# Optimization experiments

Measured on AMD Instinct MI355X. Metric: run time of the kernel, lower is better.

## Reference

```python
import jax, jax.numpy as jnp
import numpy as np

B, T, C, H, N = 4, 4096, 1024, 16, 64
D_DECAY, D_AAA, D_MV, D_GATE = 64, 64, 32, 160
EPS_GN = 1e-5 * 8 ** 2  # GroupNorm eps = 1e-5 * head_size_divisor**2


def _k(i):
    return jax.random.fold_in(jax.random.key(0), i)


def setup_inputs():
    p = {}
    p["x"] = jax.random.normal(_k(1), (B, T, C), jnp.float32)
    p["v_first"] = jax.random.normal(_k(2), (B, T, C), jnp.float32)
    for i, name in enumerate(["x_r", "x_w", "x_k", "x_v", "x_a", "x_g"]):
        p[name] = jax.random.uniform(_k(10 + i), (1, 1, C), jnp.float32)
    p["w0"] = jnp.linspace(-7.0, -2.0, C, dtype=jnp.float32).reshape(1, 1, C) + 0.5
    p["w1"] = jax.random.normal(_k(20), (C, D_DECAY), jnp.float32) * 0.02
    p["w2"] = jax.random.normal(_k(21), (D_DECAY, C), jnp.float32) * 0.02
    p["a0"] = jax.random.normal(_k(22), (1, 1, C), jnp.float32) * 0.02
    p["a1"] = jax.random.normal(_k(23), (C, D_AAA), jnp.float32) * 0.02
    p["a2"] = jax.random.normal(_k(24), (D_AAA, C), jnp.float32) * 0.02
    p["v0"] = jnp.ones((1, 1, C), jnp.float32)
    p["v1"] = jax.random.normal(_k(25), (C, D_MV), jnp.float32) * 0.02
    p["v2"] = jax.random.normal(_k(26), (D_MV, C), jnp.float32) * 0.02
    p["g1"] = jax.random.normal(_k(27), (C, D_GATE), jnp.float32) * 0.02
    p["g2"] = jax.random.normal(_k(28), (D_GATE, C), jnp.float32) * 0.02
    p["k_k"] = jnp.full((1, 1, C), 0.85, jnp.float32)
    p["k_a"] = jnp.ones((1, 1, C), jnp.float32)
    p["r_k"] = jax.random.normal(_k(29), (H, N), jnp.float32) * 0.02
    s = 0.5 / C ** 0.5
    p["Wr"] = jax.random.uniform(_k(30), (C, C), jnp.float32, -s, s)
    p["Wk"] = jax.random.uniform(_k(31), (C, C), jnp.float32, -0.1 * s, 0.1 * s)
    p["Wv"] = jax.random.uniform(_k(32), (C, C), jnp.float32, -s, s)
    p["Wo"] = jax.random.uniform(_k(33), (C, C), jnp.float32, -s, s)
    p["ln_w"] = jnp.ones((C,), jnp.float32)
    p["ln_b"] = jnp.zeros((C,), jnp.float32)
    p["alpha"] = jnp.array(0.5, jnp.float32)
    return p


def _wkv_scan(ins, reverse):
    # ins: tuple of time-major (T,B,H,N) arrays: r, decay, k, v, a, b
    def step(S, inp):
        r_t, d_t, k_t, v_t, a_t, b_t = inp
        sa = jnp.einsum('bhij,bhj->bhi', S, a_t)  # in-context removal term
        S = (S * d_t[:, :, None, :]
             + sa[..., None] * b_t[:, :, None, :]
             + v_t[..., None] * k_t[:, :, None, :])
        return S, jnp.einsum('bhij,bhj->bhi', S, r_t)
    S0 = jnp.zeros((B, H, N, N), jnp.float32)
    return jax.lax.scan(step, S0, ins, reverse=reverse)[1]


def reference(x, v_first, x_r, x_w, x_k, x_v, x_a, x_g, w0, w1, w2, a0, a1, a2,
              v0, v1, v2, g1, g2, k_k, k_a, r_k, Wr, Wk, Wv, Wo, ln_w, ln_b, alpha):
    xx = jnp.pad(x, ((0, 0), (1, 0), (0, 0)))[:, :T, :] - x  # token shift
    xr = x + xx * x_r
    xw = x + xx * x_w
    xk = x + xx * x_k
    xv = x + xx * x_v
    xa = x + xx * x_a
    xg = x + xx * x_g
    r = xr @ Wr.T
    w = -jax.nn.softplus(-(w0 + jnp.tanh(xw @ w1) @ w2)) - 0.5
    k = xk @ Wk.T
    v = xv @ Wv.T
    v = v + (v_first - v) * jax.nn.sigmoid(v0 + (xv @ v1) @ v2)  # layer_id != 0
    a = jax.nn.sigmoid(a0 + (xa @ a1) @ a2)
    g = jax.nn.sigmoid(xg @ g1) @ g2
    kk = (k * k_k).reshape(B, T, H, N)
    kk = kk / jnp.maximum(jnp.linalg.norm(kk, axis=-1, keepdims=True), 1e-12)
    k = k * (1.0 + (a - 1.0) * k_a)
    rh = r.reshape(B, T, H, N)
    kh = k.reshape(B, T, H, N)
    vh = v.reshape(B, T, H, N)
    dec = jnp.exp(-jnp.exp(w.reshape(B, T, H, N)))  # per-channel decay
    ah = -kk
    bh = kk * a.reshape(B, T, H, N)
    tm = lambda z: jnp.transpose(z, (1, 0, 2, 3))  # -> (T,B,H,N)
    ins = (tm(rh), tm(dec), tm(kh), tm(vh), tm(ah), tm(bh))
    y_f = _wkv_scan(ins, reverse=False)
    y_b = _wkv_scan(ins, reverse=True)
    y = alpha * y_f + (1.0 - alpha) * y_b  # bidirectional blend (alpha)
    y = jnp.transpose(y, (1, 0, 2, 3))  # (B,T,H,N)
    mu = y.mean(-1, keepdims=True)
    var = y.var(-1, keepdims=True)
    y = (y - mu) / jnp.sqrt(var + EPS_GN)  # GroupNorm(H groups)
    y = y * ln_w.reshape(1, 1, H, N) + ln_b.reshape(1, 1, H, N)
    y = y + (rh * kh * r_k).sum(-1, keepdims=True) * vh
    out = (y.reshape(B, T, C) * g) @ Wo.T
    return (out, v_first)
```

## Files before the change

kernel.cpp:

```cpp
#include <hip/hip_runtime.h>
#include <hip/hip_bf16.h>
#include <math.h>

#define BB 4
#define TT 4096
#define CC 1024
#define HH 16
#define NN 64
#define BT (BB*TT)
#define EPS_GN 6.4e-4f
#define TMAX (TT-1)
#define LCH 64
#define CB 8
#define NB 8
#define STR 68
#define STR2 36

typedef __attribute__((ext_vector_type(8))) short bf16x8;
typedef __attribute__((ext_vector_type(4))) float f32x4;

__device__ __forceinline__ float sigmoidf_(float x) {
    return 1.0f / (1.0f + expf(-x));
}

__device__ __forceinline__ float waveReduceSum(float v) {
    #pragma unroll
    for (int off = 32; off > 0; off >>= 1)
        v += __shfl_xor(v, off, 64);
    return v;
}

__device__ __forceinline__ unsigned short f2bf(float f) {
    unsigned u = __float_as_uint(f);
    u += 0x7FFFu + ((u >> 16) & 1u);
    return (unsigned short)(u >> 16);
}
__device__ __forceinline__ float bf2f(unsigned short h) {
    return __uint_as_float(((unsigned)h) << 16);
}

__device__ __forceinline__ void gll16(const unsigned short* g, unsigned short* l) {
    __builtin_amdgcn_global_load_lds(
        (__attribute__((address_space(1))) void*)(g),
        (__attribute__((address_space(3))) void*)(l), 16, 0, 0);
}

template<int SA0,int SA1,int SB0,int SB1>
__device__ __forceinline__ void gemm64(const float* __restrict__ A,
                                       const float* __restrict__ B,
                                       float acc[4][4], int tr, int tc) {
    #pragma unroll 2
    for (int kx = 0; kx < 64; kx += 4) {
        float a_[4][4];
        if (SA0 == 1) {
            #pragma unroll
            for (int kk = 0; kk < 4; kk++) {
                float4 t = *(const float4*)&A[tr + (kx + kk) * SA1];
                a_[0][kk] = t.x; a_[1][kk] = t.y; a_[2][kk] = t.z; a_[3][kk] = t.w;
            }
        } else {
            #pragma unroll
            for (int r = 0; r < 4; r++) {
                float4 t = *(const float4*)&A[(tr + r) * SA0 + kx];
                a_[r][0] = t.x; a_[r][1] = t.y; a_[r][2] = t.z; a_[r][3] = t.w;
            }
        }
        float b_[4][4];
        if (SB0 == 1) {
            #pragma unroll
            for (int kk = 0; kk < 4; kk++) {
                float4 t = *(const float4*)&B[tc + (kx + kk) * SB1];
                b_[0][kk] = t.x; b_[1][kk] = t.y; b_[2][kk] = t.z; b_[3][kk] = t.w;
            }
        } else {
            #pragma unroll
            for (int cq = 0; cq < 4; cq++) {
                float4 t = *(const float4*)&B[(tc + cq) * SB0 + kx];
                b_[cq][0] = t.x; b_[cq][1] = t.y; b_[cq][2] = t.z; b_[cq][3] = t.w;
            }
        }
        #pragma unroll
        for (int r = 0; r < 4; r++)
            #pragma unroll
            for (int cq = 0; cq < 4; cq++)
                #pragma unroll
                for (int kk = 0; kk < 4; kk++)
                    acc[r][cq] = fmaf(a_[r][kk], b_[cq][kk], acc[r][cq]);
    }
}

__global__ __launch_bounds__(256) void conv_split_x3(
    const float* __restrict__ X,
    const float* __restrict__ mr, const float* __restrict__ mk,
    const float* __restrict__ mv,
    unsigned short* __restrict__ rH, unsigned short* __restrict__ rL,
    unsigned short* __restrict__ kH, unsigned short* __restrict__ kL,
    unsigned short* __restrict__ vH, unsigned short* __restrict__ vL)
{
    int g = blockIdx.x * 256 + threadIdx.x;
    int m = g >> 7;
    int k = (g & 127) * 8;
    const float* px = X + (size_t)m * CC + k;
    float xv8[8], pv[8];
    {
        float4 x0 = *(const float4*)px;
        float4 x1 = *(const float4*)(px + 4);
        xv8[0]=x0.x; xv8[1]=x0.y; xv8[2]=x0.z; xv8[3]=x0.w;
        xv8[4]=x1.x; xv8[5]=x1.y; xv8[6]=x1.z; xv8[7]=x1.w;
    }
    if ((m & (TT - 1)) == 0) {
        #pragma unroll
        for (int j = 0; j < 8; j++) pv[j] = 0.f;
    } else {
        float4 p0 = *(const float4*)(px - CC);
        float4 p1 = *(const float4*)(px - CC + 4);
        pv[0]=p0.x; pv[1]=p0.y; pv[2]=p0.z; pv[3]=p0.w;
        pv[4]=p1.x; pv[5]=p1.y; pv[6]=p1.z; pv[7]=p1.w;
    }
    const float* mixes[3] = {mr, mk, mv};
    unsigned short* His[3] = {rH, kH, vH};
    unsigned short* Los[3] = {rL, kL, vL};
    #pragma unroll
    for (int s = 0; s < 3; s++) {
        float4 m0 = *(const float4*)(mixes[s] + k);
        float4 m1 = *(const float4*)(mixes[s] + k + 4);
        float mv8[8] = {m0.x,m0.y,m0.z,m0.w,m1.x,m1.y,m1.z,m1.w};
        unsigned short hi[8], lo[8];
        #pragma unroll
        for (int j = 0; j < 8; j++) {
            float a = xv8[j] + (pv[j] - xv8[j]) * mv8[j];
            hi[j] = f2bf(a);
            lo[j] = f2bf(a - bf2f(hi[j]));
        }
        uint4 H, L;
        H.x = (unsigned)hi[0] | ((unsigned)hi[1] << 16);
        H.y = (unsigned)hi[2] | ((unsigned)hi[3] << 16);
        H.z = (unsigned)hi[4] | ((unsigned)hi[5] << 16);
        H.w = (unsigned)hi[6] | ((unsigned)hi[7] << 16);
        L.x = (unsigned)lo[0] | ((unsigned)lo[1] << 16);
        L.y = (unsigned)lo[2] | ((unsigned)lo[3] << 16);
        L.z = (unsigned)lo[4] | ((unsigned)lo[5] << 16);
        L.w = (unsigned)lo[6] | ((unsigned)lo[7] << 16);
        *(uint4*)(His[s] + (size_t)g * 8) = H;
        *(uint4*)(Los[s] + (size_t)g * 8) = L;
    }
}

__global__ __launch_bounds__(256) void conv_w4(
    const float* __restrict__ Wr, const float* __restrict__ Wk,
    const float* __restrict__ Wv, const float* __restrict__ Wo,
    unsigned short* __restrict__ Hi, unsigned short* __restrict__ Lo)
{
    int g = blockIdx.x * 256 + threadIdx.x;
    int y = blockIdx.y;
    const float* W = (y == 0) ? Wr : (y == 1) ? Wk : (y == 2) ? Wv : Wo;
    size_t doff = (size_t)y * CC * CC;
    int m = g >> 7;
    int k = (g & 127) * 8;
    const float* px = W + (size_t)m * CC + k;
    float a[8];
    {
        float4 x0 = *(const float4*)px;
        float4 x1 = *(const float4*)(px + 4);
        a[0]=x0.x; a[1]=x0.y; a[2]=x0.z; a[3]=x0.w;
        a[4]=x1.x; a[5]=x1.y; a[6]=x1.z; a[7]=x1.w;
    }
    unsigned short hi[8], lo[8];
    #pragma unroll
    for (int j = 0; j < 8; j++) {
        hi[j] = f2bf(a[j]);
        lo[j] = f2bf(a[j] - bf2f(hi[j]));
    }
    uint4 H, L;
    H.x = (unsigned)hi[0] | ((unsigned)hi[1] << 16);
    H.y = (unsigned)hi[2] | ((unsigned)hi[3] << 16);
    H.z = (unsigned)hi[4] | ((unsigned)hi[5] << 16);
    H.w = (unsigned)hi[6] | ((unsigned)hi[7] << 16);
    L.x = (unsigned)lo[0] | ((unsigned)lo[1] << 16);
    L.y = (unsigned)lo[2] | ((unsigned)lo[3] << 16);
    L.z = (unsigned)lo[4] | ((unsigned)lo[5] << 16);
    L.w = (unsigned)lo[6] | ((unsigned)lo[7] << 16);
    *(uint4*)(Hi + doff + (size_t)g * 8) = H;
    *(uint4*)(Lo + doff + (size_t)g * 8) = L;
}

__global__ __launch_bounds__(256) void conv_w2(
    const float* __restrict__ W, int K, int Kp,
    unsigned short* __restrict__ Hi, unsigned short* __restrict__ Lo)
{
    int idx = blockIdx.x * 256 + threadIdx.x;
    int nk8 = Kp >> 3;
    if (idx >= CC * nk8) return;
    int n = idx / nk8, k0 = (idx - n * nk8) * 8;
    unsigned short h8[8], l8[8];
    #pragma unroll
    for (int j = 0; j < 8; j++) {
        int k = k0 + j;
        float v = (k < K) ? W[(size_t)k * CC + n] : 0.f;
        h8[j] = f2bf(v);
        l8[j] = f2bf(v - bf2f(h8[j]));
    }
    uint4 H, L;
    H.x = (unsigned)h8[0] | ((unsigned)h8[1] << 16);
    H.y = (unsigned)h8[2] | ((unsigned)h8[3] << 16);
    H.z = (unsigned)h8[4] | ((unsigned)h8[5] << 16);
    H.w = (unsigned)h8[6] | ((unsigned)h8[7] << 16);
    L.x = (unsigned)l8[0] | ((unsigned)l8[1] << 16);
    L.y = (unsigned)l8[2] | ((unsigned)l8[3] << 16);
    L.z = (unsigned)l8[4] | ((unsigned)l8[5] << 16);
    L.w = (unsigned)l8[6] | ((unsigned)l8[7] << 16);
    *(uint4*)(Hi + (size_t)n * Kp + k0) = H;
    *(uint4*)(Lo + (size_t)n * Kp + k0) = L;
}

__global__ __launch_bounds__(256, 3) void gemm_split_bf16(
    const unsigned short* __restrict__ A0h, const unsigned short* __restrict__ A0l,
    const unsigned short* __restrict__ A1h, const unsigned short* __restrict__ A1l,
    const unsigned short* __restrict__ A2h, const unsigned short* __restrict__ A2l,
    const unsigned short* __restrict__ W4h, const unsigned short* __restrict__ W4l,
    float* __restrict__ O0, float* __restrict__ O1, float* __restrict__ O2,
    int wbase)
{
    __shared__ __align__(16) unsigned short lds[4][128 * 32];
    const int sel = blockIdx.y;
    const unsigned short* Ah = (sel == 0) ? A0h : (sel == 1) ? A1h : A2h;
    const unsigned short* Al = (sel == 0) ? A0l : (sel == 1) ? A1l : A2l;
    float* Out = (sel == 0) ? O0 : (sel == 1) ? O1 : O2;
    const unsigned short* Bh = W4h + (size_t)(wbase + sel) * CC * CC;
    const unsigned short* Bl = W4l + (size_t)(wbase + sel) * CC * CC;
    const int tid = threadIdx.x, lane = tid & 63, wave = tid >> 6;
    const int wm = (wave >> 1) * 64, wn = (wave & 1) * 64;
    const int wg = blockIdx.x;
    const int xcd = wg & 7;
    const int j = wg >> 3;
    const int m0 = ((j >> 3) * 8 + xcd) * 128;
    const int n0 = (j & 7) * 128;

    f32x4 acc[4][4];
    #pragma unroll
    for (int i = 0; i < 4; i++)
        #pragma unroll
        for (int jj = 0; jj < 4; jj++)
            acc[i][jj] = (f32x4){0.f, 0.f, 0.f, 0.f};

    for (int k0 = 0; k0 < CC; k0 += 32) {
        #pragma unroll
        for (int p = 0; p < 4; p++) {
            const unsigned short* sbase = (p == 0) ? Ah : (p == 1) ? Al
                                        : (p == 2) ? Bh : Bl;
            const int rbase = (p < 2) ? m0 : n0;
            #pragma unroll
            for (int i = 0; i < 2; i++) {
                int slot = i * 256 + wave * 64 + lane;
                int row = slot >> 2, gsl = slot & 3;
                const unsigned short* src = sbase
                    + (size_t)(rbase + row) * CC + k0 + ((gsl ^ (row & 3)) * 8);
                gll16(src, &lds[p][(size_t)(i * 256 + wave * 64) * 8]);
            }
        }
        __syncthreads();

        const int gk = lane >> 4;
        bf16x8 bhf[4], blf[4];
        #pragma unroll
        for (int nt = 0; nt < 4; nt++) {
            int col = wn + nt * 16 + (lane & 15);
            int el = col * 32 + ((gk ^ (col & 3)) * 8);
            bhf[nt] = *(const bf16x8*)&lds[2][el];
            blf[nt] = *(const bf16x8*)&lds[3][el];
        }
        #pragma unroll
        for (int mt = 0; mt < 4; mt++) {
            int row = wm + mt * 16 + (lane & 15);
            int el = row * 32 + ((gk ^ (row & 3)) * 8);
            bf16x8 ahf = *(const bf16x8*)&lds[0][el];
            bf16x8 alf = *(const bf16x8*)&lds[1][el];
            #pragma unroll
            for (int nt = 0; nt < 4; nt++) {
                acc[mt][nt] = __builtin_amdgcn_mfma_f32_16x16x32_bf16(
                    ahf, bhf[nt], acc[mt][nt], 0, 0, 0);
                acc[mt][nt] = __builtin_amdgcn_mfma_f32_16x16x32_bf16(
                    alf, bhf[nt], acc[mt][nt], 0, 0, 0);
                acc[mt][nt] = __builtin_amdgcn_mfma_f32_16x16x32_bf16(
                    ahf, blf[nt], acc[mt][nt], 0, 0, 0);
            }
        }
        __syncthreads();
    }
    #pragma unroll
    for (int mt = 0; mt < 4; mt++)
        #pragma unroll
        for (int nt = 0; nt < 4; nt++) {
            int col = n0 + wn + nt * 16 + (lane & 15);
            #pragma unroll
            for (int r = 0; r < 4; r++) {
                int row = m0 + wm + mt * 16 + (lane >> 4) * 4 + r;
                Out[(size_t)row * CC + col] = acc[mt][nt][r];
            }
        }
}

__global__ __launch_bounds__(256) void lora1_all(
    const float* __restrict__ X,
    const float* __restrict__ w1, const float* __restrict__ a1,
    const float* __restrict__ v1, const float* __restrict__ g1,
    const float* __restrict__ xw, const float* __restrict__ xa,
    const float* __restrict__ xv, const float* __restrict__ xg,
    unsigned short* __restrict__ awh, unsigned short* __restrict__ awl,
    unsigned short* __restrict__ aah, unsigned short* __restrict__ aal,
    unsigned short* __restrict__ avh, unsigned short* __restrict__ avl,
    unsigned short* __restrict__ agh, unsigned short* __restrict__ agl)
{
    const int y = blockIdx.y;
    const float* W; const float* mix; unsigned short *Hi, *Lo;
    int Ncols, n0, epi, Kp;
    if (y == 0)      { W=w1; mix=xw; Hi=awh; Lo=awl; Ncols=64;  n0=0;          epi=1; Kp=64;  }
    else if (y == 1) { W=a1; mix=xa; Hi=aah; Lo=aal; Ncols=64;  n0=0;          epi=0; Kp=64;  }
    else if (y == 2) { W=v1; mix=xv; Hi=avh; Lo=avl; Ncols=32;  n0=0;          epi=0; Kp=64;  }
    else             { W=g1; mix=xg; Hi=agh; Lo=agl; Ncols=160; n0=(y-3)*64;   epi=2; Kp=192; }

    __shared__ float As[8][64];
    __shared__ float Bs[8][64];
    const int tid = threadIdx.x;
    const int m0 = blockIdx.x * 64;
    const int sr  = tid >> 1;
    const int skq = (tid & 1) * 4;
    const int t2  = tid - 128;
    const int bkr = t2 >> 4;
    const int bnq = (t2 & 15) * 4;
    const int tm = (tid >> 3) * 2;
    const int tn = (tid & 7) * 8;

    float acc[2][8];
    #pragma unroll
    for (int i = 0; i < 2; i++)
        #pragma unroll
        for (int j = 0; j < 8; j++) acc[i][j] = 0.f;

    auto ldAm = [&](int gm, int gk) -> float4 {
        const float* px = X + (size_t)gm * CC + gk;
        float4 xvv = *(const float4*)px;
        float4 pv;
        if ((gm & (TT - 1)) == 0) pv = make_float4(0.f, 0.f, 0.f, 0.f);
        else pv = *(const float4*)(px - CC);
        float4 mv = *(const float4*)(mix + gk);
        xvv.x += (pv.x - xvv.x) * mv.x;
        xvv.y += (pv.y - xvv.y) * mv.y;
        xvv.z += (pv.z - xvv.z) * mv.z;
        xvv.w += (pv.w - xvv.w) * mv.w;
        return xvv;
    };

    float4 aR = make_float4(0.f, 0.f, 0.f, 0.f);
    float4 bR = make_float4(0.f, 0.f, 0.f, 0.f);
    if (tid < 128) {
        aR = ldAm(m0 + sr, skq);
    } else {
        int gn = n0 + bnq;
        bR = (gn < Ncols) ? *(const float4*)(W + (size_t)bkr * Ncols + gn)
                          : make_float4(0.f, 0.f, 0.f, 0.f);
    }

    for (int k0 = 0; k0 < CC; k0 += 8) {
        __syncthreads();
        if (tid < 128) {
            As[skq + 0][sr] = aR.x;
            As[skq + 1][sr] = aR.y;
            As[skq + 2][sr] = aR.z;
            As[skq + 3][sr] = aR.w;
        } else {
            *(float4*)&Bs[bkr][bnq] = bR;
        }
        __syncthreads();

        if (k0 + 8 < CC) {
            if (tid < 128) {
                aR = ldAm(m0 + sr, k0 + 8 + skq);
            } else {
                int gn = n0 + bnq;
                bR = (gn < Ncols) ? *(const float4*)(W + (size_t)(k0 + 8 + bkr) * Ncols + gn)
                                  : make_float4(0.f, 0.f, 0.f, 0.f);
            }
        }

        #pragma unroll
        for (int kk = 0; kk < 8; ++kk) {
            float av[2], bv[8];
            av[0] = As[kk][tm];
            av[1] = As[kk][tm + 1];
            *(float4*)&bv[0] = *(const float4*)&Bs[kk][tn];
            *(float4*)&bv[4] = *(const float4*)&Bs[kk][tn + 4];
            #pragma unroll
            for (int i = 0; i < 2; i++)
                #pragma unroll
                for (int j = 0; j < 8; j++)
                    acc[i][j] = fmaf(av[i], bv[j], acc[i][j]);
        }
    }

    #pragma unroll
    for (int i = 0; i < 2; i++) {
        int gm = m0 + tm + i;
        int gn = n0 + tn;
        if (gn < Kp) {
            unsigned short h8[8], l8[8];
            #pragma unroll
            for (int j = 0; j < 8; j++) {
                float v = 0.f;
                if (gn + j < Ncols) {
                    v = acc[i][j];
                    if (epi == 1) v = tanhf(v);
                    else if (epi == 2) v = sigmoidf_(v);
                }
                h8[j] = f2bf(v);
                l8[j] = f2bf(v - bf2f(h8[j]));
            }
            uint4 H, L;
            H.x = (unsigned)h8[0] | ((unsigned)h8[1] << 16);
            H.y = (unsigned)h8[2] | ((unsigned)h8[3] << 16);
            H.z = (unsigned)h8[4] | ((unsigned)h8[5] << 16);
            H.w = (unsigned)h8[6] | ((unsigned)h8[7] << 16);
            L.x = (unsigned)l8[0] | ((unsigned)l8[1] << 16);
            L.y = (unsigned)l8[2] | ((unsigned)l8[3] << 16);
            L.z = (unsigned)l8[4] | ((unsigned)l8[5] << 16);
            L.w = (unsigned)l8[6] | ((unsigned)l8[7] << 16);
            *(uint4*)(Hi + (size_t)gm * Kp + gn) = H;
            *(uint4*)(Lo + (size_t)gm * Kp + gn) = L;
        }
    }
}

__global__ __launch_bounds__(256, 3) void lora2_mfma(
    const unsigned short* __restrict__ awh, const unsigned short* __restrict__ awl,
    const unsigned short* __restrict__ aah, const unsigned short* __restrict__ aal,
    const unsigned short* __restrict__ avh, const unsigned short* __restrict__ avl,
    const unsigned short* __restrict__ agh, const unsigned short* __restrict__ agl,
    const unsigned short* __restrict__ w2h, const unsigned short* __restrict__ w2l,
    const unsigned short* __restrict__ a2h, const unsigned short* __restrict__ a2l,
    const unsigned short* __restrict__ v2h, const unsigned short* __restrict__ v2l,
    const unsigned short* __restrict__ g2h, const unsigned short* __restrict__ g2l,
    const float* __restrict__ w0, const float* __restrict__ a0v,
    const float* __restrict__ v0v, const float* __restrict__ v_first,
    float* __restrict__ decb, float* __restrict__ ab,
    float* __restrict__ vbuf, float* __restrict__ gb)
{
    __shared__ __align__(16) unsigned short lds[24576];
    const int z = blockIdx.z;
    const unsigned short *Ah, *Al, *Bh, *Bl; int Kp;
    if (z == 0)      { Ah = awh; Al = awl; Bh = w2h; Bl = w2l; Kp = 64;  }
    else if (z == 1) { Ah = aah; Al = aal; Bh = a2h; Bl = a2l; Kp = 64;  }
    else if (z == 2) { Ah = avh; Al = avl; Bh = v2h; Bl = v2l; Kp = 64;  }
    else             { Ah = agh; Al = agl; Bh = g2h; Bl = g2l; Kp = 192; }

    const int tid = threadIdx.x, lane = tid & 63, wave = tid >> 6;
    const int wm = (wave >> 1) * 64, wn = (wave & 1) * 32;
    const int m0 = blockIdx.x * 128, n0 = blockIdx.y * 64;

    f32x4 acc[4][2];
    #pragma unroll
    for (int i = 0; i < 4; i++)
        #pragma unroll
        for (int jj = 0; jj < 2; jj++)
            acc[i][jj] = (f32x4){0.f, 0.f, 0.f, 0.f};

    for (int k0 = 0; k0 < Kp; k0 += 64) {
        #pragma unroll
        for (int p = 0; p < 2; p++) {
            const unsigned short* sbase = (p == 0) ? Ah : Al;
            #pragma unroll
            for (int i = 0; i < 4; i++) {
                int slot = i * 256 + wave * 64 + lane;
                int row = slot >> 3, gsl = slot & 7;
                const unsigned short* src = sbase
                    + (size_t)(m0 + row) * Kp + k0 + ((gsl ^ (row & 7)) * 8);
                gll16(src, &lds[(size_t)(p * 8192) + (size_t)(i * 256 + wave * 64) * 8]);
            }
        }
        #pragma unroll
        for (int p = 0; p < 2; p++) {
            const unsigned short* sbase = (p == 0) ? Bh : Bl;
            #pragma unroll
            for (int i = 0; i < 2; i++) {
                int slot = i * 256 + wave * 64 + lane;
                int row = slot >> 3, gsl = slot & 7;
                const unsigned short* src = sbase
                    + (size_t)(n0 + row) * Kp + k0 + ((gsl ^ (row & 7)) * 8);
                gll16(src, &lds[(size_t)(16384 + p * 4096) + (size_t)(i * 256 + wave * 64) * 8]);
            }
        }
        __syncthreads();

        #pragma unroll
        for (int ks = 0; ks < 2; ks++) {
            bf16x8 bhf[2], blf[2];
            #pragma unroll
            for (int nt = 0; nt < 2; nt++) {
                int col = wn + nt * 16 + (lane & 15);
                int gk = ks * 4 + (lane >> 4);
                int el = col * 64 + ((gk ^ (col & 7)) * 8);
                bhf[nt] = *(const bf16x8*)&lds[16384 + el];
                blf[nt] = *(const bf16x8*)&lds[20480 + el];
            }
            #pragma unroll
            for (int mt = 0; mt < 4; mt++) {
                int row = wm + mt * 16 + (lane & 15);
                int gk = ks * 4 + (lane >> 4);
                int el = row * 64 + ((gk ^ (row & 7)) * 8);
                bf16x8 ahf = *(const bf16x8*)&lds[el];
                bf16x8 alf = *(const bf16x8*)&lds[8192 + el];
                #pragma unroll
                for (int nt = 0; nt < 2; nt++) {
                    acc[mt][nt] = __builtin_amdgcn_mfma_f32_16x16x32_bf16(
                        ahf, bhf[nt], acc[mt][nt], 0, 0, 0);
                    acc[mt][nt] = __builtin_amdgcn_mfma_f32_16x16x32_bf16(
                        alf, bhf[nt], acc[mt][nt], 0, 0, 0);
                    acc[mt][nt] = __builtin_amdgcn_mfma_f32_16x16x32_bf16(
                        ahf, blf[nt], acc[mt][nt], 0, 0, 0);
                }
            }
        }
        __syncthreads();
    }
    float* cf = (float*)&lds[0];
    #pragma unroll
    for (int mt = 0; mt < 4; mt++)
        #pragma unroll
        for (int nt = 0; nt < 2; nt++)
            #pragma unroll
            for (int r = 0; r < 4; r++) {
                int row = wm + mt * 16 + (lane >> 4) * 4 + r;
                int col = wn + nt * 16 + (lane & 15);
                cf[row * 68 + col] = acc[mt][nt][r];
            }
    __syncthreads();
    #pragma unroll
    for (int i = 0; i < 8; i++) {
        int idx = tid + 256 * i;
        int row = idx >> 4, c4 = (idx & 15) * 4;
        float4 v = *(float4*)&cf[row * 68 + c4];
        int gm = m0 + row;
        int c = n0 + c4;
        size_t off = (size_t)gm * CC + c;
        if (z == 0) {
            float4 w0q = *(const float4*)(w0 + c);
            float4 o;
            o.x = expf(-expf(-log1pf(expf(-(w0q.x + v.x))) - 0.5f));
            o.y = expf(-expf(-log1pf(expf(-(w0q.y + v.y))) - 0.5f));
            o.z = expf(-expf(-log1pf(expf(-(w0q.z + v.z))) - 0.5f));
            o.w = expf(-expf(-log1pf(expf(-(w0q.w + v.w))) - 0.5f));
            *(float4*)&decb[off] = o;
        } else if (z == 1) {
            float4 a0q = *(const float4*)(a0v + c);
            float4 o;
            o.x = sigmoidf_(a0q.x + v.x);
            o.y = sigmoidf_(a0q.y + v.y);
            o.z = sigmoidf_(a0q.z + v.z);
            o.w = sigmoidf_(a0q.w + v.w);
            *(float4*)&ab[off] = o;
        } else if (z == 2) {
            float4 v0q = *(const float4*)(v0v + c);
            float4 vr = *(const float4*)&vbuf[off];
            float4 vf = *(const float4*)&v_first[off];
            float4 o;
            o.x = vr.x + (vf.x - vr.x) * sigmoidf_(v0q.x + v.x);
            o.y = vr.y + (vf.y - vr.y) * sigmoidf_(v0q.y + v.y);
            o.z = vr.z + (vf.z - vr.z) * sigmoidf_(v0q.z + v.z);
            o.w = vr.w + (vf.w - vr.w) * sigmoidf_(v0q.w + v.w);
            *(float4*)&vbuf[off] = o;
        } else {
            *(float4*)&gb[off] = v;
        }
    }
}

__global__ __launch_bounds__(256, 3) void wkvA(
    const float* __restrict__ kb, const float* __restrict__ ab,
    const float* __restrict__ vb, const float* __restrict__ decb,
    const float* __restrict__ k_k, const float* __restrict__ k_a,
    float* __restrict__ Gb, float* __restrict__ Ub,
    float* __restrict__ Bpb, float* __restrict__ Kpb,
    float* __restrict__ wcb, int cb)
{
// ... 308 lines not shown
    #pragma unroll
    for (int i = 0; i < 16; i++) {
        int p = seg * 16 + i;
        sO[lane * STR + p] = Kpb[gbase + p * 64 + lane];
    }
    __syncthreads();
    {
        float acc[4][4] = {};
        gemm64<1, STR, 1, STR>(sR, sO, acc, tr, tc);
        #pragma unroll
        for (int r = 0; r < 4; r++)
            #pragma unroll
            for (int cq = 0; cq < 4; cq++)
                sT2[(tr + r) * STR + tc + cq] = (tc + cq <= tr + r) ? acc[r][cq] : 0.f;
    }
    __syncthreads();
    #pragma unroll
    for (int i = 0; i < 16; i++) {
        int p = seg * 16 + i;
        int t = dir ? (TMAX - (c64 + p)) : (c64 + p);
        sO[p * STR + lane] = vb[((size_t)(b * TT + t)) * CC + h * 64 + lane];
    }
    __syncthreads();
    gemm64<STR, 1, 1, STR>(sT2, sO, accO, tr, tc);
    __syncthreads();
    for (int i = tid; i < 4096; i += 256)
        sO[(i >> 6) * STR + (i & 63)] = S0b[gbase + i];
    __syncthreads();
    gemm64<1, STR, STR, 1>(sR, sO, accO, tr, tc);
    #pragma unroll
    for (int r = 0; r < 4; r++) {
        int p = tr + r;
        int t = dir ? (TMAX - (c64 + p)) : (c64 + p);
        float* yp = &yb[((size_t)(b * TT + t)) * CC + h * 64 + tc];
        float4 o;
        if (first) {
            o.x = wscale * accO[r][0];
            o.y = wscale * accO[r][1];
            o.z = wscale * accO[r][2];
            o.w = wscale * accO[r][3];
        } else {
            float4 old = *(float4*)yp;
            o.x = old.x + wscale * accO[r][0];
            o.y = old.y + wscale * accO[r][1];
            o.z = old.z + wscale * accO[r][2];
            o.w = old.w + wscale * accO[r][3];
        }
        *(float4*)yp = o;
    }
}

__global__ __launch_bounds__(256) void post_kernel(
    const float* __restrict__ yb, const float* __restrict__ rbv,
    const float* __restrict__ kbv, const float* __restrict__ abv,
    const float* __restrict__ vbv, const float* __restrict__ gbv,
    const float* __restrict__ kaw, const float* __restrict__ r_k,
    const float* __restrict__ ln_w, const float* __restrict__ ln_b,
    unsigned short* __restrict__ zh, unsigned short* __restrict__ zl)
{
    const int t = blockIdx.x;
    const int tid = threadIdx.x;
    const size_t base = (size_t)t * CC;
    #pragma unroll
    for (int j = 0; j < 4; j++) {
        int c = tid + 256 * j;
        float y = yb[base + c];
        float s1 = waveReduceSum(y);
        float s2 = waveReduceSum(y * y);
        float mu = s1 * (1.0f / 64.0f);
        float var = s2 * (1.0f / 64.0f) - mu * mu;
        float yn = (y - mu) * rsqrtf(var + EPS_GN);
        yn = yn * ln_w[c] + ln_b[c];
        float rv = rbv[base + c];
        float kf = kbv[base + c] * (1.0f + (abv[base + c] - 1.0f) * kaw[c]);
        float vv = vbv[base + c];
        float dot = waveReduceSum(rv * kf * r_k[c]);
        yn += dot * vv;
        float z = yn * gbv[base + c];
        unsigned short h = f2bf(z);
        zh[base + c] = h;
        zl[base + c] = f2bf(z - bf2f(h));
    }
}

extern "C" void kernel_launch(void* const* d_in, const int* in_sizes, int n_in,
                              void* d_out, int out_size, void* d_ws, size_t ws_size,
                              hipStream_t stream)
{
    (void)in_sizes; (void)n_in; (void)out_size; (void)ws_size;
    const float* x      = (const float*)d_in[0];
    const float* vfirst = (const float*)d_in[1];
    const float* x_r    = (const float*)d_in[2];
    const float* x_w    = (const float*)d_in[3];
    const float* x_k    = (const float*)d_in[4];
    const float* x_v    = (const float*)d_in[5];
    const float* x_a    = (const float*)d_in[6];
    const float* x_g    = (const float*)d_in[7];
    const float* w0     = (const float*)d_in[8];
    const float* w1     = (const float*)d_in[9];
    const float* w2     = (const float*)d_in[10];
    const float* a0     = (const float*)d_in[11];
    const float* a1     = (const float*)d_in[12];
    const float* a2     = (const float*)d_in[13];
    const float* v0     = (const float*)d_in[14];
    const float* v1     = (const float*)d_in[15];
    const float* v2     = (const float*)d_in[16];
    const float* g1     = (const float*)d_in[17];
    const float* g2     = (const float*)d_in[18];
    const float* k_k    = (const float*)d_in[19];
    const float* k_a    = (const float*)d_in[20];
    const float* r_k    = (const float*)d_in[21];
    const float* Wr     = (const float*)d_in[22];
    const float* Wk     = (const float*)d_in[23];
    const float* Wv     = (const float*)d_in[24];
    const float* Wo     = (const float*)d_in[25];
    const float* ln_w   = (const float*)d_in[26];
    const float* ln_b   = (const float*)d_in[27];
    const float* alpha  = (const float*)d_in[28];

    const size_t SZ = (size_t)BT * CC;
    const size_t CHB = (size_t)1024 * 4096;
    float* ws   = (float*)d_ws;
    float* rb   = ws + 0 * SZ;
    float* kb   = ws + 1 * SZ;
    float* vb   = ws + 2 * SZ;
    float* decb = ws + 3 * SZ;
    float* ab   = ws + 4 * SZ;
    float* actf = ws + 5 * SZ;
    unsigned short* awh = (unsigned short*)actf;
    unsigned short* awl = awh + (size_t)BT * 64;
    unsigned short* aah = awl + (size_t)BT * 64;
    unsigned short* aal = aah + (size_t)BT * 64;
    unsigned short* avh = aal + (size_t)BT * 64;
    unsigned short* avl = avh + (size_t)BT * 64;
    unsigned short* agh = avl + (size_t)BT * 64;
    unsigned short* agl = agh + (size_t)BT * 192;
    float* Gb   = actf + (size_t)BT * 384;
    float* Ub   = Gb + CHB;
    float* Bpb  = Ub + CHB;
    float* Kpb  = Bpb + CHB;
    float* S0b  = Kpb + CHB;
    float* wcb  = S0b + CHB;
    float* Scur = wcb + CHB;
    unsigned short* W4h = (unsigned short*)(Scur + (size_t)128 * 4096);
    unsigned short* W4l = W4h + (size_t)CC * CC * 4;
    unsigned short* w2th = W4l + (size_t)CC * CC * 4;
    unsigned short* w2tl = w2th + (size_t)CC * 64;
    unsigned short* a2th = w2tl + (size_t)CC * 64;
    unsigned short* a2tl = a2th + (size_t)CC * 64;
    unsigned short* v2th = a2tl + (size_t)CC * 64;
    unsigned short* v2tl = v2th + (size_t)CC * 64;
    unsigned short* g2th = v2tl + (size_t)CC * 64;
    unsigned short* g2tl = g2th + (size_t)CC * 192;
    float* outp = (float*)d_out;
    unsigned short* xrh = (unsigned short*)outp;
    unsigned short* xrl = xrh + SZ;
    unsigned short* xkh = xrl + SZ;
    unsigned short* xkl = xkh + SZ;
    unsigned short* xvh = (unsigned short*)decb;
    unsigned short* xvl = xvh + SZ;
    float* gb   = outp;
    float* yb   = outp + SZ;
    unsigned short* zAh = (unsigned short*)decb;
    unsigned short* zAl = zAh + SZ;

    dim3 blk(256);
    const int NG_A = BT * (CC / 8);
    dim3 gridA(NG_A / 256);

    conv_split_x3<<<gridA, blk, 0, stream>>>(x, x_r, x_k, x_v,
                                             xrh, xrl, xkh, xkl, xvh, xvl);
    conv_w4<<<dim3(512, 4), blk, 0, stream>>>(Wr, Wk, Wv, Wo, W4h, W4l);
    gemm_split_bf16<<<dim3(1024, 3), blk, 0, stream>>>(
        xrh, xrl, xkh, xkl, xvh, xvl, W4h, W4l, rb, kb, vb, 0);

    conv_w2<<<dim3(32), blk, 0, stream>>>(w2, 64, 64, w2th, w2tl);
    conv_w2<<<dim3(32), blk, 0, stream>>>(a2, 64, 64, a2th, a2tl);
    conv_w2<<<dim3(32), blk, 0, stream>>>(v2, 32, 64, v2th, v2tl);
    conv_w2<<<dim3(96), blk, 0, stream>>>(g2, 160, 192, g2th, g2tl);

    lora1_all<<<dim3(BT / 64, 6), blk, 0, stream>>>(x, w1, a1, v1, g1,
        x_w, x_a, x_v, x_g, awh, awl, aah, aal, avh, avl, agh, agl);
    lora2_mfma<<<dim3(BT / 128, CC / 64, 4), blk, 0, stream>>>(
        awh, awl, aah, aal, avh, avl, agh, agl,
        w2th, w2tl, a2th, a2tl, v2th, v2tl, g2th, g2tl,
        w0, a0, v0, vfirst, decb, ab, vb, gb);

    hipMemsetAsync(Scur, 0, (size_t)128 * 4096 * sizeof(float), stream);
    for (int cb = 0; cb < NB; ++cb) {
        wkvA<<<dim3(1024), blk, 0, stream>>>(kb, ab, vb, decb, k_k, k_a,
                                             Gb, Ub, Bpb, Kpb, wcb, cb);
        wkvB<<<dim3(256), blk, 0, stream>>>(vb, Gb, Ub, Bpb, Kpb, wcb, S0b, Scur, cb);
        wkvC<<<dim3(1024), blk, 0, stream>>>(rb, vb, Bpb, Kpb, Ub, S0b, wcb,
                                             alpha, yb, cb);
    }

    post_kernel<<<dim3(BT), blk, 0, stream>>>(yb, rb, kb, ab, vb, gb, k_a, r_k,
                                              ln_w, ln_b, zAh, zAl);
    hipMemcpyAsync(outp + SZ, vfirst, SZ * sizeof(float),
                   hipMemcpyDeviceToDevice, stream);
    gemm_split_bf16<<<dim3(1024, 1), blk, 0, stream>>>(
        zAh, zAl, zAh, zAl, zAh, zAl, W4h, W4l, outp, outp, outp, 3);
}
```

Baseline: 3.024 ms.

## Run LoRA first-stage projections on split-bf16 MFMA with pre-split mixed inputs

Replaces the fp32 SIMT LoRA down-projection kernel with an MFMA kernel that uses hi/lo bf16 splitting (three MFMAs per tile) for near-fp32 accuracy. The token-shift mixes for w, a and g are now computed and split in the existing conversion kernel, and the LoRA weights get a new transpose-and-split kernel. The mixed inputs are staged in the r/k/v buffers, so the main projection GEMM is moved after the LoRA kernel. This removes slow scalar FMA work but adds extra memory traffic for three more split activation tensors.

```diff
diff --git a/kernel.cpp b/kernel.cpp
--- a/kernel.cpp
+++ b/kernel.cpp
@@ -89,13 +89,17 @@
     }
 }
 
-__global__ __launch_bounds__(256) void conv_split_x3(
+__global__ __launch_bounds__(256) void conv_split_x6(
     const float* __restrict__ X,
     const float* __restrict__ mr, const float* __restrict__ mk,
-    const float* __restrict__ mv,
+    const float* __restrict__ mv, const float* __restrict__ mw,
+    const float* __restrict__ ma, const float* __restrict__ mg,
     unsigned short* __restrict__ rH, unsigned short* __restrict__ rL,
     unsigned short* __restrict__ kH, unsigned short* __restrict__ kL,
-    unsigned short* __restrict__ vH, unsigned short* __restrict__ vL)
+    unsigned short* __restrict__ vH, unsigned short* __restrict__ vL,
+    unsigned short* __restrict__ wH, unsigned short* __restrict__ wL,
+    unsigned short* __restrict__ aH, unsigned short* __restrict__ aL,
+    unsigned short* __restrict__ gH, unsigned short* __restrict__ gL)
 {
     int g = blockIdx.x * 256 + threadIdx.x;
     int m = g >> 7;
@@ -117,11 +121,10 @@
         pv[0]=p0.x; pv[1]=p0.y; pv[2]=p0.z; pv[3]=p0.w;
         pv[4]=p1.x; pv[5]=p1.y; pv[6]=p1.z; pv[7]=p1.w;
     }
-    const float* mixes[3] = {mr, mk, mv};
-    unsigned short* His[3] = {rH, kH, vH};
-    unsigned short* Los[3] = {rL, kL, vL};
-    #pragma unroll
-    for (int s = 0; s < 3; s++) {
+    const float* mixes[6] = {mr, mk, mv, mw, ma, mg};
+    unsigned short* His[6] = {rH, kH, vH, wH, aH, gH};
+    unsigned short* Los[6] = {rL, kL, vL, wL, aL, gL};
+    for (int s = 0; s < 6; s++) {
         float4 m0 = *(const float4*)(mixes[s] + k);
         float4 m1 = *(const float4*)(mixes[s] + k + 4);
         float mv8[8] = {m0.x,m0.y,m0.z,m0.w,m1.x,m1.y,m1.z,m1.w};
@@ -211,6 +214,34 @@
     L.w = (unsigned)l8[6] | ((unsigned)l8[7] << 16);
     *(uint4*)(Hi + (size_t)n * Kp + k0) = H;
     *(uint4*)(Lo + (size_t)n * Kp + k0) = L;
+}
+
+__global__ __launch_bounds__(256) void conv_w1(
+    const float* __restrict__ W, int N, int Npad,
+    unsigned short* __restrict__ Hi, unsigned short* __restrict__ Lo)
+{
+    int idx = blockIdx.x * 256 + threadIdx.x;
+    if (idx >= Npad * 128) return;
+    int n = idx >> 7, k0 = (idx & 127) * 8;
+    unsigned short h8[8], l8[8];
+    #pragma unroll
+    for (int j = 0; j < 8; j++) {
+        int k = k0 + j;
+        float v = (n < N) ? W[(size_t)k * N + n] : 0.f;
+        h8[j] = f2bf(v);
+        l8[j] = f2bf(v - bf2f(h8[j]));
+    }
+    uint4 H, L;
+    H.x = (unsigned)h8[0] | ((unsigned)h8[1] << 16);
+    H.y = (unsigned)h8[2] | ((unsigned)h8[3] << 16);
+    H.z = (unsigned)h8[4] | ((unsigned)h8[5] << 16);
+    H.w = (unsigned)h8[6] | ((unsigned)h8[7] << 16);
+    L.x = (unsigned)l8[0] | ((unsigned)l8[1] << 16);
+    L.y = (unsigned)l8[2] | ((unsigned)l8[3] << 16);
+    L.z = (unsigned)l8[4] | ((unsigned)l8[5] << 16);
+    L.w = (unsigned)l8[6] | ((unsigned)l8[7] << 16);
+    *(uint4*)(Hi + (size_t)n * CC + k0) = H;
+    *(uint4*)(Lo + (size_t)n * CC + k0) = L;
 }
 
 __global__ __launch_bounds__(256, 3) void gemm_split_bf16(
@@ -300,134 +331,111 @@
         }
 }
 
-__global__ __launch_bounds__(256) void lora1_all(
-    const float* __restrict__ X,
-    const float* __restrict__ w1, const float* __restrict__ a1,
-    const float* __restrict__ v1, const float* __restrict__ g1,
-    const float* __restrict__ xw, const float* __restrict__ xa,
-    const float* __restrict__ xv, const float* __restrict__ xg,
+__global__ __launch_bounds__(256, 3) void lora1_mfma(
+    const unsigned short* __restrict__ xwh, const unsigned short* __restrict__ xwl,
+    const unsigned short* __restrict__ xah, const unsigned short* __restrict__ xal,
+    const unsigned short* __restrict__ xvh, const unsigned short* __restrict__ xvl,
+    const unsigned short* __restrict__ xgh, const unsigned short* __restrict__ xgl,
+    const unsigned short* __restrict__ w1th, const unsigned short* __restrict__ w1tl,
+    const unsigned short* __restrict__ a1th, const unsigned short* __restrict__ a1tl,
+    const unsigned short* __restrict__ v1th, const unsigned short* __restrict__ v1tl,
+    const unsigned short* __restrict__ g1th, const unsigned short* __restrict__ g1tl,
     unsigned short* __restrict__ awh, unsigned short* __restrict__ awl,
     unsigned short* __restrict__ aah, unsigned short* __restrict__ aal,
     unsigned short* __restrict__ avh, unsigned short* __restrict__ avl,
     unsigned short* __restrict__ agh, unsigned short* __restrict__ agl)
 {
+    __shared__ __align__(16) unsigned short lds[12288];
     const int y = blockIdx.y;
-    const float* W; const float* mix; unsigned short *Hi, *Lo;
-    int Ncols, n0, epi, Kp;
-    if (y == 0)      { W=w1; mix=xw; Hi=awh; Lo=awl; Ncols=64;  n0=0;          epi=1; Kp=64;  }
-    else if (y == 1) { W=a1; mix=xa; Hi=aah; Lo=aal; Ncols=64;  n0=0;          epi=0; Kp=64;  }
-    else if (y == 2) { W=v1; mix=xv; Hi=avh; Lo=avl; Ncols=32;  n0=0;          epi=0; Kp=64;  }
-    else             { W=g1; mix=xg; Hi=agh; Lo=agl; Ncols=160; n0=(y-3)*64;   epi=2; Kp=192; }
-
-    __shared__ float As[8][64];
-    __shared__ float Bs[8][64];
-    const int tid = threadIdx.x;
-    const int m0 = blockIdx.x * 64;
-    const int sr  = tid >> 1;
-    const int skq = (tid & 1) * 4;
-    const int t2  = tid - 128;
-    const int bkr = t2 >> 4;
-    const int bnq = (t2 & 15) * 4;
-    const int tm = (tid >> 3) * 2;
-    const int tn = (tid & 7) * 8;
-
-    float acc[2][8];
-    #pragma unroll
-    for (int i = 0; i < 2; i++)
-        #pragma unroll
-        for (int j = 0; j < 8; j++) acc[i][j] = 0.f;
-
-    auto ldAm = [&](int gm, int gk) -> float4 {
-        const float* px = X + (size_t)gm * CC + gk;
-        float4 xvv = *(const float4*)px;
-        float4 pv;
-        if ((gm & (TT - 1)) == 0) pv = make_float4(0.f, 0.f, 0.f, 0.f);
-        else pv = *(const float4*)(px - CC);
-        float4 mv = *(const float4*)(mix + gk);
-        xvv.x += (pv.x - xvv.x) * mv.x;
-        xvv.y += (pv.y - xvv.y) * mv.y;
-        xvv.z += (pv.z - xvv.z) * mv.z;
-        xvv.w += (pv.w - xvv.w) * mv.w;
-        return xvv;
-    };
-
-    float4 aR = make_float4(0.f, 0.f, 0.f, 0.f);
-    float4 bR = make_float4(0.f, 0.f, 0.f, 0.f);
-    if (tid < 128) {
-        aR = ldAm(m0 + sr, skq);
-    } else {
-        int gn = n0 + bnq;
-        bR = (gn < Ncols) ? *(const float4*)(W + (size_t)bkr * Ncols + gn)
-                          : make_float4(0.f, 0.f, 0.f, 0.f);
-    }
-
-    for (int k0 = 0; k0 < CC; k0 += 8) {
+    const unsigned short *Ah, *Al, *Bh, *Bl;
+    unsigned short *Oh, *Ol;
+    int n0, epi, Kp;
+    if (y == 0)      { Ah=xwh; Al=xwl; Bh=w1th; Bl=w1tl; Oh=awh; Ol=awl; n0=0; epi=1; Kp=64; }
+    else if (y == 1) { Ah=xah; Al=xal; Bh=a1th; Bl=a1tl; Oh=aah; Ol=aal; n0=0; epi=0; Kp=64; }
+    else if (y == 2) { Ah=xvh; Al=xvl; Bh=v1th; Bl=v1tl; Oh=avh; Ol=avl; n0=0; epi=0; Kp=64; }
+    else             { Ah=xgh; Al=xgl; Bh=g1th + (size_t)(y-3)*64*CC;
+                       Bl=g1tl + (size_t)(y-3)*64*CC; Oh=agh; Ol=agl;
+                       n0=(y-3)*64; epi=2; Kp=192; }
+
+    const int tid = threadIdx.x, lane = tid & 63, wave = tid >> 6;
+    const int wm = (wave >> 1) * 64, wn = (wave & 1) * 32;
+    const int m0 = blockIdx.x * 128;
+
+    f32x4 acc[4][2];
+    #pragma unroll
+    for (int i = 0; i < 4; i++)
+        #pragma unroll
+        for (int jj = 0; jj < 2; jj++)
+            acc[i][jj] = (f32x4){0.f, 0.f, 0.f, 0.f};
+
+    for (int k0 = 0; k0 < CC; k0 += 32) {
+        #pragma unroll
+        for (int p = 0; p < 2; p++) {
+            const unsigned short* sbase = (p == 0) ? Ah : Al;
+            #pragma unroll
+            for (int i = 0; i < 2; i++) {
+                int slot = i * 256 + wave * 64 + lane;
+                int row = slot >> 2, gsl = slot & 3;
+                const unsigned short* src = sbase
+                    + (size_t)(m0 + row) * CC + k0 + ((gsl ^ (row & 3)) * 8);
+                gll16(src, &lds[(size_t)(p * 4096) + (size_t)(i * 256 + wave * 64) * 8]);
+            }
+        }
+        #pragma unroll
+        for (int p = 0; p < 2; p++) {
+            const unsigned short* sbase = (p == 0) ? Bh : Bl;
+            int slot = wave * 64 + lane;
+            int row = slot >> 2, gsl = slot & 3;
+            const unsigned short* src = sbase
+                + (size_t)row * CC + k0 + ((gsl ^ (row & 3)) * 8);
+            gll16(src, &lds[(size_t)(8192 + p * 2048) + (size_t)slot * 8]);
+        }
         __syncthreads();
-        if (tid < 128) {
-            As[skq + 0][sr] = aR.x;
-            As[skq + 1][sr] = aR.y;
-            As[skq + 2][sr] = aR.z;
-            As[skq + 3][sr] = aR.w;
-        } else {
-            *(float4*)&Bs[bkr][bnq] = bR;
+
+        const int gk = lane >> 4;
+        bf16x8 bhf[2], blf[2];
+        #pragma unroll
+        for (int nt = 0; nt < 2; nt++) {
+            int col = wn + nt * 16 + (lane & 15);
+            int el = col * 32 + ((gk ^ (col & 3)) * 8);
+            bhf[nt] = *(const bf16x8*)&lds[8192 + el];
+            blf[nt] = *(const bf16x8*)&lds[10240 + el];
+        }
+        #pragma unroll
+        for (int mt = 0; mt < 4; mt++) {
+            int row = wm + mt * 16 + (lane & 15);
+            int el = row * 32 + ((gk ^ (row & 3)) * 8);
+            bf16x8 ahf = *(const bf16x8*)&lds[el];
+            bf16x8 alf = *(const bf16x8*)&lds[4096 + el];
+            #pragma unroll
+            for (int nt = 0; nt < 2; nt++) {
+                acc[mt][nt] = __builtin_amdgcn_mfma_f32_16x16x32_bf16(
+                    ahf, bhf[nt], acc[mt][nt], 0, 0, 0);
+                acc[mt][nt] = __builtin_amdgcn_mfma_f32_16x16x32_bf16(
+                    alf, bhf[nt], acc[mt][nt], 0, 0, 0);
+                acc[mt][nt] = __builtin_amdgcn_mfma_f32_16x16x32_bf16(
+                    ahf, blf[nt], acc[mt][nt], 0, 0, 0);
+            }
         }
         __syncthreads();
-
-        if (k0 + 8 < CC) {
-            if (tid < 128) {
-                aR = ldAm(m0 + sr, k0 + 8 + skq);
-            } else {
-                int gn = n0 + bnq;
-                bR = (gn < Ncols) ? *(const float4*)(W + (size_t)(k0 + 8 + bkr) * Ncols + gn)
-                                  : make_float4(0.f, 0.f, 0.f, 0.f);
-            }
-        }
-
-        #pragma unroll
-        for (int kk = 0; kk < 8; ++kk) {
-            float av[2], bv[8];
-            av[0] = As[kk][tm];
-            av[1] = As[kk][tm + 1];
-            *(float4*)&bv[0] = *(const float4*)&Bs[kk][tn];
-            *(float4*)&bv[4] = *(const float4*)&Bs[kk][tn + 4];
-            #pragma unroll
-            for (int i = 0; i < 2; i++)
-                #pragma unroll
-                for (int j = 0; j < 8; j++)
-                    acc[i][j] = fmaf(av[i], bv[j], acc[i][j]);
-        }
-    }
-
-    #pragma unroll
-    for (int i = 0; i < 2; i++) {
-        int gm = m0 + tm + i;
-        int gn = n0 + tn;
-        if (gn < Kp) {
-            unsigned short h8[8], l8[8];
-            #pragma unroll
-            for (int j = 0; j < 8; j++) {
-                float v = 0.f;
-                if (gn + j < Ncols) {
-                    v = acc[i][j];
-                    if (epi == 1) v = tanhf(v);
-                    else if (epi == 2) v = sigmoidf_(v);
-                }
-                h8[j] = f2bf(v);
-                l8[j] = f2bf(v - bf2f(h8[j]));
-            }
-            uint4 H, L;
-            H.x = (unsigned)h8[0] | ((unsigned)h8[1] << 16);
-            H.y = (unsigned)h8[2] | ((unsigned)h8[3] << 16);
-            H.z = (unsigned)h8[4] | ((unsigned)h8[5] << 16);
-            H.w = (unsigned)h8[6] | ((unsigned)h8[7] << 16);
-            L.x = (unsigned)l8[0] | ((unsigned)l8[1] << 16);
-            L.y = (unsigned)l8[2] | ((unsigned)l8[3] << 16);
-            L.z = (unsigned)l8[4] | ((unsigned)l8[5] << 16);
-            L.w = (unsigned)l8[6] | ((unsigned)l8[7] << 16);
-            *(uint4*)(Hi + (size_t)gm * Kp + gn) = H;
-            *(uint4*)(Lo + (size_t)gm * Kp + gn) = L;
-        }
-    }
+    }
+    #pragma unroll
+    for (int mt = 0; mt < 4; mt++)
+        #pragma unroll
+        for (int nt = 0; nt < 2; nt++) {
+            int col = n0 + wn + nt * 16 + (lane & 15);
+            #pragma unroll
+            for (int r = 0; r < 4; r++) {
+                int row = m0 + wm + mt * 16 + (lane >> 4) * 4 + r;
+                float v = acc[mt][nt][r];
+                if (epi == 1) v = tanhf(v);
+                else if (epi == 2) v = sigmoidf_(v);
+                unsigned short h = f2bf(v);
+                size_t off = (size_t)row * Kp + col;
+                Oh[off] = h;
+                Ol[off] = f2bf(v - bf2f(h));
+            }
+        }
 }
 
 __global__ __launch_bounds__(256, 3) void lora2_mfma(
@@ -1042,6 +1050,14 @@
     unsigned short* v2tl = v2th + (size_t)CC * 64;
     unsigned short* g2th = v2tl + (size_t)CC * 64;
     unsigned short* g2tl = g2th + (size_t)CC * 192;
+    unsigned short* w1th = g2tl + (size_t)CC * 192;
+    unsigned short* w1tl = w1th + (size_t)64 * CC;
+    unsigned short* a1th = w1tl + (size_t)64 * CC;
+    unsigned short* a1tl = a1th + (size_t)64 * CC;
+    unsigned short* v1th = a1tl + (size_t)64 * CC;
+    unsigned short* v1tl = v1th + (size_t)64 * CC;
+    unsigned short* g1th = v1tl + (size_t)64 * CC;
+    unsigned short* g1tl = g1th + (size_t)192 * CC;
     float* outp = (float*)d_out;
     unsigned short* xrh = (unsigned short*)outp;
     unsigned short* xrl = xrh + SZ;
@@ -1049,6 +1065,12 @@
     unsigned short* xkl = xkh + SZ;
     unsigned short* xvh = (unsigned short*)decb;
     unsigned short* xvl = xvh + SZ;
+    unsigned short* xwh = (unsigned short*)rb;
+    unsigned short* xwl = xwh + SZ;
+    unsigned short* xah = (unsigned short*)kb;
+    unsigned short* xal = xah + SZ;
+    unsigned short* xgh = (unsigned short*)vb;
+    unsigned short* xgl = xgh + SZ;
     float* gb   = outp;
     float* yb   = outp + SZ;
     unsigned short* zAh = (unsigned short*)decb;
@@ -1058,19 +1080,26 @@
     const int NG_A = BT * (CC / 8);
     dim3 gridA(NG_A / 256);
 
-    conv_split_x3<<<gridA, blk, 0, stream>>>(x, x_r, x_k, x_v,
-                                             xrh, xrl, xkh, xkl, xvh, xvl);
+    conv_split_x6<<<gridA, blk, 0, stream>>>(x, x_r, x_k, x_v, x_w, x_a, x_g,
+        xrh, xrl, xkh, xkl, xvh, xvl, xwh, xwl, xah, xal, xgh, xgl);
     conv_w4<<<dim3(512, 4), blk, 0, stream>>>(Wr, Wk, Wv, Wo, W4h, W4l);
-    gemm_split_bf16<<<dim3(1024, 3), blk, 0, stream>>>(
-        xrh, xrl, xkh, xkl, xvh, xvl, W4h, W4l, rb, kb, vb, 0);
-
+    conv_w1<<<dim3(32), blk, 0, stream>>>(w1, 64, 64, w1th, w1tl);
+    conv_w1<<<dim3(32), blk, 0, stream>>>(a1, 64, 64, a1th, a1tl);
+    conv_w1<<<dim3(32), blk, 0, stream>>>(v1, 32, 64, v1th, v1tl);
+    conv_w1<<<dim3(96), blk, 0, stream>>>(g1, 160, 192, g1th, g1tl);
     conv_w2<<<dim3(32), blk, 0, stream>>>(w2, 64, 64, w2th, w2tl);
     conv_w2<<<dim3(32), blk, 0, stream>>>(a2, 64, 64, a2th, a2tl);
     conv_w2<<<dim3(32), blk, 0, stream>>>(v2, 32, 64, v2th, v2tl);
     conv_w2<<<dim3(96), blk, 0, stream>>>(g2, 160, 192, g2th, g2tl);
 
-    lora1_all<<<dim3(BT / 64, 6), blk, 0, stream>>>(x, w1, a1, v1, g1,
-        x_w, x_a, x_v, x_g, awh, awl, aah, aal, avh, avl, agh, agl);
+    lora1_mfma<<<dim3(BT / 128, 6), blk, 0, stream>>>(
+        xwh, xwl, xah, xal, xvh, xvl, xgh, xgl,
+        w1th, w1tl, a1th, a1tl, v1th, v1tl, g1th, g1tl,
+        awh, awl, aah, aal, avh, avl, agh, agl);
+
+    gemm_split_bf16<<<dim3(1024, 3), blk, 0, stream>>>(
+        xrh, xrl, xkh, xkl, xvh, xvl, W4h, W4l, rb, kb, vb, 0);
+
     lora2_mfma<<<dim3(BT / 128, CC / 64, 4), blk, 0, stream>>>(
         awh, awl, aah, aal, avh, avl, agh, agl,
         w2th, w2tl, a2th, a2tl, v2th, v2tl, g2th, g2tl,
```

Result: no change. 2.969 ms (-1.8%).
